# Kernel optimization log

Measured on AMD Instinct MI355X. Metric: run time of the kernel, lower is better.

## Reference

```python
import jax, jax.numpy as jnp
import numpy as np

VOCAB = 256; EMB = 384; D_MODEL = 512; D_INNER = 1024; D_STATE = 16
D_CONV = 4; DT_RANK = 32; NL = 8; B = 2; L = 2048

def silu(x):
    return x * jax.nn.sigmoid(x)

def layernorm(x, g, b):
    mu = x.mean(-1, keepdims=True)
    v = ((x - mu) ** 2).mean(-1, keepdims=True)
    return (x - mu) / jnp.sqrt(v + 1e-5) * g + b

def conv1d_same(x, w, b, pad):
    # x: (B, C, L), w: (O, I, K)
    out = jax.lax.conv_general_dilated(x, w, (1,), [(pad, pad)],
                                       dimension_numbers=('NCH', 'OIH', 'NCH'))
    return out + b[None, :, None]

def mamba_layer(x, in_w, cw, cb, xp_w, dt_w, dt_b, A_log, Dp, out_w):
    # x: (B, L, D_MODEL)
    xz = x @ in_w.T                      # (B, L, 2*D_INNER)
    xi, z = xz[..., :D_INNER], xz[..., D_INNER:]
    # causal depthwise conv over time
    xi_t = xi.transpose(0, 2, 1)         # (B, D_INNER, L)
    xc = jax.lax.conv_general_dilated(xi_t, cw[:, None, :], (1,), [(D_CONV - 1, 0)],
                                      dimension_numbers=('NCH', 'OIH', 'NCH'),
                                      feature_group_count=D_INNER)
    xc = silu(xc + cb[None, :, None]).transpose(0, 2, 1)   # (B, L, D_INNER)
    dbc = xc @ xp_w.T                    # (B, L, DT_RANK + 2*D_STATE)
    dt = jax.nn.softplus(dbc[..., :DT_RANK] @ dt_w.T + dt_b)   # (B, L, D_INNER)
    Bm = dbc[..., DT_RANK:DT_RANK + D_STATE]                    # (B, L, D_STATE)
    Cm = dbc[..., DT_RANK + D_STATE:]                           # (B, L, D_STATE)
    A = -jnp.exp(A_log)                                         # (D_INNER, D_STATE)
    dA = jnp.exp(dt[..., None] * A)                             # (B, L, D_INNER, D_STATE)
    dBx = (dt * xc)[..., None] * Bm[:, :, None, :]              # (B, L, D_INNER, D_STATE)

    def step(h, inp):
        a, bx, c = inp
        h = a * h + bx                                          # (B, D_INNER, D_STATE)
        return h, jnp.einsum('bds,bs->bd', h, c)

    h0 = jnp.zeros((x.shape[0], D_INNER, D_STATE), x.dtype)
    _, ys = jax.lax.scan(step, h0, (dA.transpose(1, 0, 2, 3),
                                    dBx.transpose(1, 0, 2, 3),
                                    Cm.transpose(1, 0, 2)))
    y = ys.transpose(1, 0, 2) + Dp * xc                         # (B, L, D_INNER)
    y = y * silu(z)
    return y @ out_w.T

def setup_inputs() -> dict:
    key = jax.random.key(0)
    ks = jax.random.split(key, 24)
    s = 0.02
    inp = {
        'tokens': jax.random.randint(ks[0], (B, L), 0, VOCAB),
        'emb': jax.random.normal(ks[1], (VOCAB, EMB)) * s,
        'conv1_w': jax.random.normal(ks[2], (512, EMB, 5)) * s,
        'conv1_b': jnp.zeros((512,)),
        'ln1_g': jnp.ones((512,)), 'ln1_b': jnp.zeros((512,)),
        'conv2_w': jax.random.normal(ks[3], (512, 512, 3)) * s,
        'conv2_b': jnp.zeros((512,)),
        'ln2_g': jnp.ones((512,)), 'ln2_b': jnp.zeros((512,)),
        'pos_emb': jax.random.normal(ks[4], (L, D_MODEL)) * s,
        'in_proj_w': jax.random.normal(ks[5], (NL, 2 * D_INNER, D_MODEL)) * s,
        'conv_w': jax.random.normal(ks[6], (NL, D_INNER, D_CONV)) * s,
        'conv_b': jnp.zeros((NL, D_INNER)),
        'x_proj_w': jax.random.normal(ks[7], (NL, DT_RANK + 2 * D_STATE, D_INNER)) * s,
        'dt_proj_w': jax.random.normal(ks[8], (NL, D_INNER, DT_RANK)) * s,
        'dt_proj_b': jnp.full((NL, D_INNER), -4.0),
        'A_log': jnp.log(jnp.tile(jnp.arange(1, D_STATE + 1, dtype=jnp.float32),
                                  (NL, D_INNER, 1))),
        'D': jnp.ones((NL, D_INNER)),
        'out_proj_w': jax.random.normal(ks[9], (NL, D_MODEL, D_INNER)) * s,
        'fc_w': jax.random.normal(ks[10], (VOCAB, D_MODEL)) * s,
        'fc_b': jnp.zeros((VOCAB,)),
    }
    return inp

def reference(tokens, emb, conv1_w, conv1_b, ln1_g, ln1_b, conv2_w, conv2_b,
              ln2_g, ln2_b, pos_emb, in_proj_w, conv_w, conv_b, x_proj_w,
              dt_proj_w, dt_proj_b, A_log, D, out_proj_w, fc_w, fc_b):
    x = emb[tokens]                                   # (B, L, EMB)
    # CNN frontend (GELU + channel LayerNorm, dropout=0 in eval)
    x = x.transpose(0, 2, 1)
    x = jax.nn.gelu(conv1d_same(x, conv1_w, conv1_b, 2), approximate=False)
    x = layernorm(x.transpose(0, 2, 1), ln1_g, ln1_b).transpose(0, 2, 1)
    x = jax.nn.gelu(conv1d_same(x, conv2_w, conv2_b, 1), approximate=False)
    x = layernorm(x.transpose(0, 2, 1), ln2_g, ln2_b)  # (B, L, 512)
    x = x + pos_emb[None, :x.shape[1]]
    for i in range(NL):
        x = mamba_layer(x, in_proj_w[i], conv_w[i], conv_b[i], x_proj_w[i],
                        dt_proj_w[i], dt_proj_b[i], A_log[i], D[i], out_proj_w[i])
    rep = x[:, -1, :]
    return rep @ fc_w.T + fc_b
```

## Files before the change

### kernel.cpp

```cpp
#include <hip/hip_runtime.h>
#include <hip/hip_bf16.h>
#include <math.h>

#define VOCABN 256
#define EMBN   384
#define DM     512
#define DI     1024
#define DSTATE 16
#define DCONVN 4
#define DTRANK 32
#define NLAYER 8
#define BBATCH 2
#define LSEQ   2048
#define MROWS  (BBATCH*LSEQ)
#define SCHUNK 64
#define NCHUNK (LSEQ/SCHUNK)

typedef short s8v  __attribute__((ext_vector_type(8)));
typedef float f32x4 __attribute__((ext_vector_type(4)));

__device__ __forceinline__ ushort f2bf(float f) {
    uint u = __float_as_uint(f);
    return (ushort)((u + 0x7fffu + ((u >> 16) & 1u)) >> 16);
}
__device__ __forceinline__ float bf2f(ushort h) {
    return __uint_as_float((uint)h << 16);
}
__device__ __forceinline__ uint packbf(float f) {
    ushort h = f2bf(f);
    ushort l = f2bf(f - bf2f(h));
    return ((uint)h << 16) | (uint)l;
}
__device__ __forceinline__ void unp4(uint4 p, ushort* hdst, ushort* ldst) {
    ushort4 h, l;
    h.x = (ushort)(p.x >> 16); l.x = (ushort)(p.x & 0xffffu);
    h.y = (ushort)(p.y >> 16); l.y = (ushort)(p.y & 0xffffu);
    h.z = (ushort)(p.z >> 16); l.z = (ushort)(p.z & 0xffffu);
    h.w = (ushort)(p.w >> 16); l.w = (ushort)(p.w & 0xffffu);
    *(ushort4*)hdst = h; *(ushort4*)ldst = l;
}

__global__ void pack3_kernel(const float* __restrict__ a, int na,
                             const float* __restrict__ b, int nb,
                             const float* __restrict__ c, int nc,
                             uint* __restrict__ pa, uint* __restrict__ pb, uint* __restrict__ pc) {
    int i = blockIdx.x * 256 + threadIdx.x;
    if (i < na) pa[i] = packbf(a[i]);
    else if (i < na + nb) pb[i - na] = packbf(b[i - na]);
    else if (i < na + nb + nc) pc[i - na - nb] = packbf(c[i - na - nb]);
}

template<int CI, int CK>
__global__ void pack_convw_kernel(const float* __restrict__ w, uint* __restrict__ pw) {
    int idx = blockIdx.x * 256 + threadIdx.x;
    if (idx >= 512 * CI * CK) return;
    int k  = idx % CK;
    int ci = (idx / CK) % CI;
    int co = idx / (CK * CI);
    pw[((size_t)(k * 512) + co) * CI + ci] = packbf(w[idx]);
}

__global__ void embed_kernel(const int* __restrict__ tok, const float* __restrict__ emb,
                             uint* __restrict__ px0) {
    int idx = blockIdx.x * 256 + threadIdx.x;
    int c = idx % EMBN;
    int t = idx / EMBN;
    px0[idx] = packbf(emb[tok[t] * EMBN + c]);
}

__device__ __forceinline__ float gelu_exact(float x) {
    return 0.5f * x * (1.f + erff(x * 0.70710678118654752f));
}

template<int CI, int CK, int PAD>
__global__ __launch_bounds__(256) void conv_mfma_kernel(
    const uint* __restrict__ PA, const uint* __restrict__ PW,
    const float* __restrict__ bias, float* __restrict__ out)
{
    constexpr int ROWS = 128 + CK - 1;
    const int t0  = blockIdx.x * 128;
    const int co0 = blockIdx.y * 32;
    const int tid = threadIdx.x;
    const int wid = tid >> 6, lane = tid & 63;
    const int rb = wid * 32;
    const int lr = lane & 15, lk = (lane >> 4) * 8;
    const int bstart = (t0 / LSEQ) * LSEQ;

    __shared__ alignas(16) ushort Ah[ROWS][40], Al[ROWS][40];
    __shared__ alignas(16) ushort Bh[CK][32][40], Bl[CK][32][40];

    f32x4 acc[2][2];
#pragma unroll
    for (int m = 0; m < 2; m++)
#pragma unroll
        for (int n = 0; n < 2; n++) acc[m][n] = (f32x4){0.f, 0.f, 0.f, 0.f};

    for (int ci0 = 0; ci0 < CI; ci0 += 32) {
        __syncthreads();
        for (int idx = tid; idx < ROWS * 8; idx += 256) {
            int r = idx >> 3, c4 = (idx & 7) * 4;
            int g = t0 - PAD + r;
            uint4 v = make_uint4(0u, 0u, 0u, 0u);
            if (g >= bstart && g < bstart + LSEQ)
                v = *(const uint4*)&PA[(size_t)g * CI + ci0 + c4];
            unp4(v, &Ah[r][c4], &Al[r][c4]);
        }
        for (int idx = tid; idx < CK * 32 * 8; idx += 256) {
            int k = idx >> 8;
            int r = (idx >> 3) & 31;
            int c4 = (idx & 7) * 4;
            uint4 v = *(const uint4*)&PW[((size_t)(k * 512) + co0 + r) * CI + ci0 + c4];
            unp4(v, &Bh[k][r][c4], &Bl[k][r][c4]);
        }
        __syncthreads();

#pragma unroll
        for (int k = 0; k < CK; k++) {
            s8v ah[2], al[2], bh[2], bl[2];
#pragma unroll
            for (int m = 0; m < 2; m++) {
                ah[m] = *(const s8v*)&Ah[rb + m * 16 + lr + k][lk];
                al[m] = *(const s8v*)&Al[rb + m * 16 + lr + k][lk];
            }
#pragma unroll
            for (int n = 0; n < 2; n++) {
                bh[n] = *(const s8v*)&Bh[k][n * 16 + lr][lk];
                bl[n] = *(const s8v*)&Bl[k][n * 16 + lr][lk];
            }
#pragma unroll
            for (int m = 0; m < 2; m++)
#pragma unroll
                for (int n = 0; n < 2; n++) {
                    acc[m][n] = __builtin_amdgcn_mfma_f32_16x16x32_bf16(ah[m], bh[n], acc[m][n], 0, 0, 0);
                    acc[m][n] = __builtin_amdgcn_mfma_f32_16x16x32_bf16(ah[m], bl[n], acc[m][n], 0, 0, 0);
                    acc[m][n] = __builtin_amdgcn_mfma_f32_16x16x32_bf16(al[m], bh[n], acc[m][n], 0, 0, 0);
                }
        }
    }

#pragma unroll
    for (int m = 0; m < 2; m++)
#pragma unroll
        for (int n = 0; n < 2; n++) {
            int gcol = co0 + n * 16 + lr;
            float bv = bias[gcol];
#pragma unroll
            for (int r = 0; r < 4; r++) {
                int grow = t0 + rb + m * 16 + (lane >> 4) * 4 + r;
                out[(size_t)grow * 512 + gcol] = gelu_exact(acc[m][n][r] + bv);
            }
        }
}

template<bool ADDPOS, bool PACK>
__global__ __launch_bounds__(256) void ln_kernel(
    const float* __restrict__ in, const float* __restrict__ g, const float* __restrict__ bb,
    const float* __restrict__ pos, float* __restrict__ out, uint* __restrict__ pout)
{
    int row  = blockIdx.x * 4 + (threadIdx.x >> 6);
    int lane = threadIdx.x & 63;
    const float* xr = in + (size_t)row * DM;
    float v[8];
    float s = 0.f;
#pragma unroll
    for (int i = 0; i < 8; i++) { v[i] = xr[lane + i * 64]; s += v[i]; }
#pragma unroll
    for (int o = 32; o >= 1; o >>= 1) s += __shfl_xor(s, o);
    float mu = s * (1.f / 512.f);
    float var = 0.f;
#pragma unroll
    for (int i = 0; i < 8; i++) { float d = v[i] - mu; var = fmaf(d, d, var); }
#pragma unroll
    for (int o = 32; o >= 1; o >>= 1) var += __shfl_xor(var, o);
    var *= (1.f / 512.f);
    float rstd = rsqrtf(var + 1e-5f);
    int t = row & (LSEQ - 1);
#pragma unroll
    for (int i = 0; i < 8; i++) {
        int c = lane + i * 64;
        float o = (v[i] - mu) * rstd * g[c] + bb[c];
        if (ADDPOS) o += pos[t * DM + c];
        if (PACK) pout[(size_t)row * DM + c] = packbf(o);
        else      out [(size_t)row * DM + c] = o;
    }
}

template<int EPI>
__global__ __launch_bounds__(256) void gemm_kernel(
    const float* __restrict__ A, int lda,
    const float* __restrict__ Wm,
    const float* __restrict__ bias,
    float* __restrict__ C, int N, int K)
{
    const int m0 = blockIdx.x * 64;
    const int n0 = blockIdx.y * 64;
    const int tid = threadIdx.x;
    const int tx = tid & 15, ty = tid >> 4;

    __shared__ float As[16][64];
    __shared__ float Ws[16][64];

    float acc[4][4];
#pragma unroll
    for (int i = 0; i < 4; i++)
#pragma unroll
        for (int j = 0; j < 4; j++) acc[i][j] = 0.f;

    const int am = tid >> 2;
    const int ak = (tid & 3) * 4;

    for (int k0 = 0; k0 < K; k0 += 16) {
        float4 av = *(const float4*)&A[(size_t)(m0 + am) * lda + k0 + ak];
        float4 wv = *(const float4*)&Wm[(size_t)(n0 + am) * K + k0 + ak];
        __syncthreads();
        As[ak + 0][am] = av.x; As[ak + 1][am] = av.y; As[ak + 2][am] = av.z; As[ak + 3][am] = av.w;
        Ws[ak + 0][am] = wv.x; Ws[ak + 1][am] = wv.y; Ws[ak + 2][am] = wv.z; Ws[ak + 3][am] = wv.w;
        __syncthreads();
#pragma unroll
        for (int kk = 0; kk < 16; kk++) {
            float4 a = *(const float4*)&As[kk][ty * 4];
            float4 w = *(const float4*)&Ws[kk][tx * 4];
            acc[0][0] = fmaf(a.x, w.x, acc[0][0]); acc[0][1] = fmaf(a.x, w.y, acc[0][1]);
            acc[0][2] = fmaf(a.x, w.z, acc[0][2]); acc[0][3] = fmaf(a.x, w.w, acc[0][3]);
            acc[1][0] = fmaf(a.y, w.x, acc[1][0]); acc[1][1] = fmaf(a.y, w.y, acc[1][1]);
            acc[1][2] = fmaf(a.y, w.z, acc[1][2]); acc[1][3] = fmaf(a.y, w.w, acc[1][3]);
            acc[2][0] = fmaf(a.z, w.x, acc[2][0]); acc[2][1] = fmaf(a.z, w.y, acc[2][1]);
            acc[2][2] = fmaf(a.z, w.z, acc[2][2]); acc[2][3] = fmaf(a.z, w.w, acc[2][3]);
            acc[3][0] = fmaf(a.w, w.x, acc[3][0]); acc[3][1] = fmaf(a.w, w.y, acc[3][1]);
            acc[3][2] = fmaf(a.w, w.z, acc[3][2]); acc[3][3] = fmaf(a.w, w.w, acc[3][3]);
        }
    }

#pragma unroll
    for (int i = 0; i < 4; i++) {
        float4 o;
        float r[4];
#pragma unroll
        for (int j = 0; j < 4; j++) {
            float v = acc[i][j];
            if (EPI == 1) {
                v += bias[n0 + tx * 4 + j];
                v = fmaxf(v, 0.f) + log1pf(expf(-fabsf(v)));
            }
            r[j] = v;
        }
        o.x = r[0]; o.y = r[1]; o.z = r[2]; o.w = r[3];
        *(float4*)&C[(size_t)(m0 + ty * 4 + i) * N + n0 + tx * 4] = o;
    }
}

template<int BN, int EPI>
__global__ __launch_bounds__(256) void gemm_mfma_p(
    const uint* __restrict__ PA, int lda,
    const uint* __restrict__ PW,
    float* __restrict__ C, uint* __restrict__ PC, int N, int K)
{
    constexpr int MR = (BN == 128) ? 4 : 2;
    constexpr int NR = 4;
    const int m0 = blockIdx.x * 128;
    const int n0 = blockIdx.y * BN;
    const int tid = threadIdx.x;
    const int wid = tid >> 6;
    const int lane = tid & 63;
    const int rb = (BN == 128) ? (wid >> 1) * 64 : wid * 32;
    const int cb = (BN == 128) ? (wid & 1) * 64 : 0;
    const int lr = lane & 15;
    const int lk = (lane >> 4) * 8;

    __shared__ alignas(16) ushort Ah[128][40], Al[128][40];
    __shared__ alignas(16) ushort Bh[BN][40],  Bl[BN][40];

    f32x4 acc[MR][NR];
#pragma unroll
    for (int m = 0; m < MR; m++)
#pragma unroll
        for (int n = 0; n < NR; n++) acc[m][n] = (f32x4){0.f, 0.f, 0.f, 0.f};

    const int srow = tid >> 3;
    const int scol = (tid & 7) * 4;

    for (int k0 = 0; k0 < K; k0 += 32) {
        uint4 av[4], wv[BN / 32];
#pragma unroll
        for (int i = 0; i < 4; i++)
            av[i] = *(const uint4*)&PA[(size_t)(m0 + srow + 32 * i) * lda + k0 + scol];
#pragma unroll
        for (int i = 0; i < BN / 32; i++)
            wv[i] = *(const uint4*)&PW[(size_t)(n0 + srow + 32 * i) * K + k0 + scol];

        __syncthreads();
#pragma unroll
        for (int i = 0; i < 4; i++)
            unp4(av[i], &Ah[srow + 32 * i][scol], &Al[srow + 32 * i][scol]);
#pragma unroll
        for (int i = 0; i < BN / 32; i++)
            unp4(wv[i], &Bh[srow + 32 * i][scol], &Bl[srow + 32 * i][scol]);
        __syncthreads();

        s8v ah[MR], al[MR], bh[NR], bl[NR];
#pragma unroll
        for (int m = 0; m < MR; m++) {
            ah[m] = *(const s8v*)&Ah[rb + m * 16 + lr][lk];
            al[m] = *(const s8v*)&Al[rb + m * 16 + lr][lk];
        }
#pragma unroll
        for (int n = 0; n < NR; n++) {
            bh[n] = *(const s8v*)&Bh[cb + n * 16 + lr][lk];
            bl[n] = *(const s8v*)&Bl[cb + n * 16 + lr][lk];
        }
#pragma unroll
        for (int m = 0; m < MR; m++)
#pragma unroll
            for (int n = 0; n < NR; n++) {
                acc[m][n] = __builtin_amdgcn_mfma_f32_16x16x32_bf16(ah[m], bh[n], acc[m][n], 0, 0, 0);
                acc[m][n] = __builtin_amdgcn_mfma_f32_16x16x32_bf16(ah[m], bl[n], acc[m][n], 0, 0, 0);
                acc[m][n] = __builtin_amdgcn_mfma_f32_16x16x32_bf16(al[m], bh[n], acc[m][n], 0, 0, 0);
            }
    }

#pragma unroll
    for (int m = 0; m < MR; m++)
#pragma unroll
        for (int n = 0; n < NR; n++) {
#pragma unroll
            for (int r = 0; r < 4; r++) {
                int grow = m0 + rb + m * 16 + (lane >> 4) * 4 + r;
                int gcol = n0 + cb + n * 16 + lr;
                float v = acc[m][n][r];
                C[(size_t)grow * N + gcol] = v;
                if (EPI == 2) PC[(size_t)grow * N + gcol] = packbf(v);
            }
        }
}

__global__ void dwconv_silu_kernel(const float* __restrict__ xz, const float* __restrict__ cw,
                                   const float* __restrict__ cb, float* __restrict__ xc,
                                   uint* __restrict__ pxc) {
    int idx = blockIdx.x * 256 + threadIdx.x;
    int d = idx & (DI - 1);
    int r = idx >> 10;
    int tl = r & (LSEQ - 1);
    float acc = cb[d];
#pragma unroll
    for (int k = 0; k < DCONVN; k++) {
        int ts = tl - 3 + k;
        if (ts >= 0) acc = fmaf(xz[(size_t)(r - 3 + k) * (2 * DI) + d], cw[d * DCONVN + k], acc);
    }
    float sig = 1.f / (1.f + expf(-acc));
    float v = acc * sig;
    xc[idx] = v;
    pxc[idx] = packbf(v);
}

__global__ __launch_bounds__(256) void scan_local_kernel(
    const float* __restrict__ dt, const float* __restrict__ xc,
    const float* __restrict__ dbc, const float* __restrict__ A_log,
    float* __restrict__ S, float* __restrict__ P)
{
    const int sg = threadIdx.x & 3;
    const int dl = threadIdx.x >> 2;
    const int dq = blockIdx.x & 15;
    const int c  = (blockIdx.x >> 4) & (NCHUNK - 1);
    const int b  = blockIdx.x >> 9;
    const int d  = dq * 64 + dl;

    float4 alog = *(const float4*)&A_log[d * DSTATE + sg * 4];
    float Av[4];
    Av[0] = -expf(alog.x) * 1.44269504f;
    Av[1] = -expf(alog.y) * 1.44269504f;
    Av[2] = -expf(alog.z) * 1.44269504f;
    Av[3] = -expf(alog.w) * 1.44269504f;

    float h[4] = {0.f, 0.f, 0.f, 0.f};
    float sumdt = 0.f;
    const int rowbase = b * LSEQ + c * SCHUNK;

#pragma unroll 4
    for (int t = 0; t < SCHUNK; t++) {
        int r = rowbase + t;
        float dtv = dt[(size_t)r * DI + d];
        float xcv = xc[(size_t)r * DI + d];
        float4 Bv = *(const float4*)&dbc[(size_t)r * 64 + DTRANK + sg * 4];
        float dx = dtv * xcv;
        h[0] = fmaf(exp2f(dtv * Av[0]), h[0], dx * Bv.x);
        h[1] = fmaf(exp2f(dtv * Av[1]), h[1], dx * Bv.y);
        h[2] = fmaf(exp2f(dtv * Av[2]), h[2], dx * Bv.z);
        h[3] = fmaf(exp2f(dtv * Av[3]), h[3], dx * Bv.w);
        sumdt += dtv;
    }
    size_t off = ((size_t)(b * NCHUNK + c) * DI + d) * DSTATE + sg * 4;
    *(float4*)&S[off] = make_float4(h[0], h[1], h[2], h[3]);
    *(float4*)&P[off] = make_float4(exp2f(Av[0] * sumdt), exp2f(Av[1] * sumdt),
                                    exp2f(Av[2] * sumdt), exp2f(Av[3] * sumdt));
}

__global__ __launch_bounds__(256) void scan_combine_kernel(
    const float* __restrict__ S, const float* __restrict__ P, float* __restrict__ H)
{
    int idx = blockIdx.x * 256 + threadIdx.x;
    int b = idx >> 14;
    int rem = idx & 16383;
    float h = 0.f;
#pragma unroll
    for (int c = 0; c < NCHUNK; c++) {
        size_t off = ((size_t)(b * NCHUNK + c) * DI) * DSTATE + rem;
        H[off] = h;
        h = fmaf(P[off], h, S[off]);
    }
}

__global__ __launch_bounds__(256) void scan_out_kernel(
    const float* __restrict__ dt, const float* __restrict__ xc,
    const float* __restrict__ dbc, const float* __restrict__ xz,
    const float* __restrict__ A_log, const float* __restrict__ Dp,
    const float* __restrict__ H, uint* __restrict__ py)
{
    const int sg = threadIdx.x & 3;
    const int dl = threadIdx.x >> 2;
    const int dq = blockIdx.x & 15;
    const int c  = (blockIdx.x >> 4) & (NCHUNK - 1);
    const int b  = blockIdx.x >> 9;
    const int d  = dq * 64 + dl;

    float4 alog = *(const float4*)&A_log[d * DSTATE + sg * 4];
    float Av[4];
    Av[0] = -expf(alog.x) * 1.44269504f;
    Av[1] = -expf(alog.y) * 1.44269504f;
    Av[2] = -expf(alog.z) * 1.44269504f;
    Av[3] = -expf(alog.w) * 1.44269504f;
    float Dval = Dp[d];

    float4 hv = *(const float4*)&H[((size_t)(b * NCHUNK + c) * DI + d) * DSTATE + sg * 4];
    float h[4] = {hv.x, hv.y, hv.z, hv.w};
    const int rowbase = b * LSEQ + c * SCHUNK;

#pragma unroll 2
    for (int t = 0; t < SCHUNK; t++) {
        int r = rowbase + t;
        float dtv = dt[(size_t)r * DI + d];
        float xcv = xc[(size_t)r * DI + d];
        float4 Bv = *(const float4*)&dbc[(size_t)r * 64 + DTRANK + sg * 4];
        float4 Cv = *(const float4*)&dbc[(size_t)r * 64 + DTRANK + DSTATE + sg * 4];
        float dx = dtv * xcv;
        h[0] = fmaf(exp2f(dtv * Av[0]), h[0], dx * Bv.x);
        h[1] = fmaf(exp2f(dtv * Av[1]), h[1], dx * Bv.y);
        h[2] = fmaf(exp2f(dtv * Av[2]), h[2], dx * Bv.z);
        h[3] = fmaf(exp2f(dtv * Av[3]), h[3], dx * Bv.w);
        float p = h[0] * Cv.x;
        p = fmaf(h[1], Cv.y, p);
        p = fmaf(h[2], Cv.z, p);
        p = fmaf(h[3], Cv.w, p);
        p += __shfl_xor(p, 1);
        p += __shfl_xor(p, 2);
        if (sg == 0) {
            float zv = xz[(size_t)r * (2 * DI) + DI + d];
            float zsig = 1.f / (1.f + exp2f(-zv * 1.44269504f));
            py[(size_t)r * DI + d] = packbf((p + Dval * xcv) * (zv * zsig));
        }
    }
}

__global__ void fc_kernel(const float* __restrict__ x, const float* __restrict__ fcw,
                          const float* __restrict__ fcb, float* __restrict__ out) {
    int b = blockIdx.x;
    int v = threadIdx.x;
    __shared__ float rep[DM];
    const float* xr = x + (size_t)(b * LSEQ + LSEQ - 1) * DM;
    for (int i = threadIdx.x; i < DM; i += 256) rep[i] = xr[i];
    __syncthreads();
    float acc = fcb[v];
    for (int k = 0; k < DM; k++) acc = fmaf(rep[k], fcw[v * DM + k], acc);
    out[b * VOCABN + v] = acc;
}

extern "C" void kernel_launch(void* const* d_in, const int* in_sizes, int n_in,
                              void* d_out, int out_size, void* d_ws, size_t ws_size,
                              hipStream_t stream) {
    const int*   tokens    = (const int*)  d_in[0];
    const float* emb       = (const float*)d_in[1];
    const float* conv1_w   = (const float*)d_in[2];
    const float* conv1_b   = (const float*)d_in[3];
    const float* ln1_g     = (const float*)d_in[4];
    const float* ln1_b     = (const float*)d_in[5];
    const float* conv2_w   = (const float*)d_in[6];
    const float* conv2_b   = (const float*)d_in[7];
    const float* ln2_g     = (const float*)d_in[8];
    const float* ln2_b     = (const float*)d_in[9];
    const float* pos_emb   = (const float*)d_in[10];
    const float* in_proj_w = (const float*)d_in[11];
    const float* conv_w    = (const float*)d_in[12];
    const float* conv_b    = (const float*)d_in[13];
    const float* x_proj_w  = (const float*)d_in[14];
    const float* dt_proj_w = (const float*)d_in[15];
    const float* dt_proj_b = (const float*)d_in[16];
    const float* A_log     = (const float*)d_in[17];
    const float* Dp_all    = (const float*)d_in[18];
    const float* out_proj_w= (const float*)d_in[19];
    const float* fc_w      = (const float*)d_in[20];
    const float* fc_b      = (const float*)d_in[21];

    float* ws = (float*)d_ws;
    float* X    = ws;
    float* T1   = X   + 2097152;
    float* XZ   = T1  + 2097152;
    float* XC   = XZ  + 8388608;
    float* DT   = XC  + 4194304;
    uint*  PY   = (uint*)(DT + 4194304);
    float* DBC  = (float*)PY + 4194304;
    uint*  PX   = (uint*)(DBC + 262144);
    uint*  PXC  = PX  + 2097152;
    uint*  PWIN = PXC + 4194304;
    uint*  PWOUT= PWIN + 1048576;
    uint*  PWX  = PWOUT + 524288;
    uint*  PX0  = (uint*)XZ;
    uint*  PWC1 = (uint*)XC;
    uint*  PWC2 = (uint*)XC + 983040;
    uint*  PB   = (uint*)DT;
    float* SCN_S = (float*)PXC;
    float* SCN_P = SCN_S + 1048576;
    float* SCN_H = SCN_P + 1048576;

    pack_convw_kernel<EMBN, 5><<<(512 * EMBN * 5 + 255) / 256, 256, 0, stream>>>(conv1_w, PWC1);
    pack_convw_kernel<DM,   3><<<(512 * DM   * 3 + 255) / 256, 256, 0, stream>>>(conv2_w, PWC2);
    embed_kernel<<<(MROWS * EMBN) / 256, 256, 0, stream>>>(tokens, emb, PX0);
    conv_mfma_kernel<EMBN, 5, 2><<<dim3(MROWS / 128, 16), 256, 0, stream>>>(PX0, PWC1, conv1_b, T1);
    ln_kernel<false, true><<<MROWS / 4, 256, 0, stream>>>(T1, ln1_g, ln1_b, nullptr, nullptr, PB);
    conv_mfma_kernel<DM, 3, 1><<<dim3(MROWS / 128, 16), 256, 0, stream>>>(PB, PWC2, conv2_b, T1);
    ln_kernel<true, true><<<MROWS / 4, 256, 0, stream>>>(T1, ln2_g, ln2_b, pos_emb, nullptr, PX);

    for (int l = 0; l < NLAYER; l++) {
        pack3_kernel<<<(2 * DI * DM + DM * DI + 64 * DI + 255) / 256, 256, 0, stream>>>(
            in_proj_w + (size_t)l * 2 * DI * DM, 2 * DI * DM,
            out_proj_w + (size_t)l * DM * DI, DM * DI,
            x_proj_w + (size_t)l * 64 * DI, 64 * DI,
            PWIN, PWOUT, PWX);
        gemm_mfma_p<128, 0><<<dim3(MROWS / 128, (2 * DI) / 128), 256, 0, stream>>>(
            PX, DM, PWIN, XZ, nullptr, 2 * DI, DM);
        dwconv_silu_kernel<<<(MROWS * DI) / 256, 256, 0, stream>>>(
            XZ, conv_w + (size_t)l * DI * DCONVN, conv_b + (size_t)l * DI, XC, PXC);
        gemm_mfma_p<64, 0><<<dim3(MROWS / 128, 1), 256, 0, stream>>>(
            PXC, DI, PWX, DBC, nullptr, 64, DI);
        gemm_kernel<1><<<dim3(MROWS / 64, DI / 64), 256, 0, stream>>>(
            DBC, 64, dt_proj_w + (size_t)l * DI * DTRANK, dt_proj_b + (size_t)l * DI, DT, DI, DTRANK);
        scan_local_kernel<<<16 * NCHUNK * BBATCH, 256, 0, stream>>>(
            DT, XC, DBC, A_log + (size_t)l * DI * DSTATE, SCN_S, SCN_P);
        scan_combine_kernel<<<(BBATCH * DI * DSTATE) / 256, 256, 0, stream>>>(
            SCN_S, SCN_P, SCN_H);
        scan_out_kernel<<<16 * NCHUNK * BBATCH, 256, 0, stream>>>(
            DT, XC, DBC, XZ, A_log + (size_t)l * DI * DSTATE, Dp_all + (size_t)l * DI,
            SCN_H, PY);
        gemm_mfma_p<64, 2><<<dim3(MROWS / 128, DM / 64), 256, 0, stream>>>(
            PY, DI, PWOUT, X, PX, DM, DI);
    }

    fc_kernel<<<BBATCH, 256, 0, stream>>>(X, fc_w, fc_b, (float*)d_out);
}
```

Measured before the change: 2.129 ms.

## Move dt projection to split-bf16 MFMA GEMM and stage scan inputs in LDS

Replaces the scalar fp32 dt_proj GEMM with the split-bf16 MFMA GEMM. Its weights are packed with the other layer weights, the x_proj output is packed as input, and bias plus softplus are fused in a new epilogue. The scan_local and scan_out kernels now preload each chunk's dt, xc and B/C rows into shared memory with vectorized loads instead of doing strided per-thread global reads each timestep. The risks are a K=32 GEMM that fits the MFMA K-loop tiling only loosely, and extra LDS use per block.

```diff
diff --git a/kernel.cpp b/kernel.cpp
--- a/kernel.cpp
+++ b/kernel.cpp
@@ -40,14 +40,17 @@
     *(ushort4*)hdst = h; *(ushort4*)ldst = l;
 }
 
-__global__ void pack3_kernel(const float* __restrict__ a, int na,
+__global__ void pack4_kernel(const float* __restrict__ a, int na,
                              const float* __restrict__ b, int nb,
                              const float* __restrict__ c, int nc,
-                             uint* __restrict__ pa, uint* __restrict__ pb, uint* __restrict__ pc) {
+                             const float* __restrict__ d, int nd,
+                             uint* __restrict__ pa, uint* __restrict__ pb,
+                             uint* __restrict__ pc, uint* __restrict__ pd) {
     int i = blockIdx.x * 256 + threadIdx.x;
     if (i < na) pa[i] = packbf(a[i]);
     else if (i < na + nb) pb[i - na] = packbf(b[i - na]);
     else if (i < na + nb + nc) pc[i - na - nb] = packbf(c[i - na - nb]);
+    else if (i < na + nb + nc + nd) pd[i - na - nb - nc] = packbf(d[i - na - nb - nc]);
 }
 
 template<int CI, int CK>
@@ -185,74 +188,11 @@
     }
 }
 
-template<int EPI>
-__global__ __launch_bounds__(256) void gemm_kernel(
-    const float* __restrict__ A, int lda,
-    const float* __restrict__ Wm,
-    const float* __restrict__ bias,
-    float* __restrict__ C, int N, int K)
-{
-    const int m0 = blockIdx.x * 64;
-    const int n0 = blockIdx.y * 64;
-    const int tid = threadIdx.x;
-    const int tx = tid & 15, ty = tid >> 4;
-
-    __shared__ float As[16][64];
-    __shared__ float Ws[16][64];
-
-    float acc[4][4];
-#pragma unroll
-    for (int i = 0; i < 4; i++)
-#pragma unroll
-        for (int j = 0; j < 4; j++) acc[i][j] = 0.f;
-
-    const int am = tid >> 2;
-    const int ak = (tid & 3) * 4;
-
-    for (int k0 = 0; k0 < K; k0 += 16) {
-        float4 av = *(const float4*)&A[(size_t)(m0 + am) * lda + k0 + ak];
-        float4 wv = *(const float4*)&Wm[(size_t)(n0 + am) * K + k0 + ak];
-        __syncthreads();
-        As[ak + 0][am] = av.x; As[ak + 1][am] = av.y; As[ak + 2][am] = av.z; As[ak + 3][am] = av.w;
-        Ws[ak + 0][am] = wv.x; Ws[ak + 1][am] = wv.y; Ws[ak + 2][am] = wv.z; Ws[ak + 3][am] = wv.w;
-        __syncthreads();
-#pragma unroll
-        for (int kk = 0; kk < 16; kk++) {
-            float4 a = *(const float4*)&As[kk][ty * 4];
-            float4 w = *(const float4*)&Ws[kk][tx * 4];
-            acc[0][0] = fmaf(a.x, w.x, acc[0][0]); acc[0][1] = fmaf(a.x, w.y, acc[0][1]);
-            acc[0][2] = fmaf(a.x, w.z, acc[0][2]); acc[0][3] = fmaf(a.x, w.w, acc[0][3]);
-            acc[1][0] = fmaf(a.y, w.x, acc[1][0]); acc[1][1] = fmaf(a.y, w.y, acc[1][1]);
-            acc[1][2] = fmaf(a.y, w.z, acc[1][2]); acc[1][3] = fmaf(a.y, w.w, acc[1][3]);
-            acc[2][0] = fmaf(a.z, w.x, acc[2][0]); acc[2][1] = fmaf(a.z, w.y, acc[2][1]);
-            acc[2][2] = fmaf(a.z, w.z, acc[2][2]); acc[2][3] = fmaf(a.z, w.w, acc[2][3]);
-            acc[3][0] = fmaf(a.w, w.x, acc[3][0]); acc[3][1] = fmaf(a.w, w.y, acc[3][1]);
-            acc[3][2] = fmaf(a.w, w.z, acc[3][2]); acc[3][3] = fmaf(a.w, w.w, acc[3][3]);
-        }
-    }
-
-#pragma unroll
-    for (int i = 0; i < 4; i++) {
-        float4 o;
-        float r[4];
-#pragma unroll
-        for (int j = 0; j < 4; j++) {
-            float v = acc[i][j];
-            if (EPI == 1) {
-                v += bias[n0 + tx * 4 + j];
-                v = fmaxf(v, 0.f) + log1pf(expf(-fabsf(v)));
-            }
-            r[j] = v;
-        }
-        o.x = r[0]; o.y = r[1]; o.z = r[2]; o.w = r[3];
-        *(float4*)&C[(size_t)(m0 + ty * 4 + i) * N + n0 + tx * 4] = o;
-    }
-}
-
 template<int BN, int EPI>
 __global__ __launch_bounds__(256) void gemm_mfma_p(
     const uint* __restrict__ PA, int lda,
     const uint* __restrict__ PW,
+    const float* __restrict__ bias,
     float* __restrict__ C, uint* __restrict__ PC, int N, int K)
 {
     constexpr int MR = (BN == 128) ? 4 : 2;
@@ -327,6 +267,10 @@
                 int grow = m0 + rb + m * 16 + (lane >> 4) * 4 + r;
                 int gcol = n0 + cb + n * 16 + lr;
                 float v = acc[m][n][r];
+                if (EPI == 3) {
+                    v += bias[gcol];
+                    v = fmaxf(v, 0.f) + log1pf(expf(-fabsf(v)));
+                }
                 C[(size_t)grow * N + gcol] = v;
                 if (EPI == 2) PC[(size_t)grow * N + gcol] = packbf(v);
             }
@@ -362,7 +306,23 @@
     const int dq = blockIdx.x & 15;
     const int c  = (blockIdx.x >> 4) & (NCHUNK - 1);
     const int b  = blockIdx.x >> 9;
-    const int d  = dq * 64 + dl;
+    const int d0 = dq * 64;
+    const int d  = d0 + dl;
+    const int rowbase = b * LSEQ + c * SCHUNK;
+
+    __shared__ float dtl[SCHUNK][68];
+    __shared__ float xcl[SCHUNK][68];
+    __shared__ float bl [SCHUNK][16];
+
+    for (int i = threadIdx.x; i < SCHUNK * 16; i += 256) {
+        int t = i >> 4, c4 = (i & 15) * 4;
+        *(float4*)&dtl[t][c4] = *(const float4*)&dt[(size_t)(rowbase + t) * DI + d0 + c4];
+        *(float4*)&xcl[t][c4] = *(const float4*)&xc[(size_t)(rowbase + t) * DI + d0 + c4];
+    }
+    for (int i = threadIdx.x; i < SCHUNK * 4; i += 256) {
+        int t = i >> 2, c4 = (i & 3) * 4;
+        *(float4*)&bl[t][c4] = *(const float4*)&dbc[(size_t)(rowbase + t) * 64 + DTRANK + c4];
+    }
 
     float4 alog = *(const float4*)&A_log[d * DSTATE + sg * 4];
     float Av[4];
@@ -373,14 +333,13 @@
 
     float h[4] = {0.f, 0.f, 0.f, 0.f};
     float sumdt = 0.f;
-    const int rowbase = b * LSEQ + c * SCHUNK;
+    __syncthreads();
 
 #pragma unroll 4
     for (int t = 0; t < SCHUNK; t++) {
-        int r = rowbase + t;
-        float dtv = dt[(size_t)r * DI + d];
-        float xcv = xc[(size_t)r * DI + d];
-        float4 Bv = *(const float4*)&dbc[(size_t)r * 64 + DTRANK + sg * 4];
+        float dtv = dtl[t][dl];
+        float xcv = xcl[t][dl];
+        float4 Bv = *(const float4*)&bl[t][sg * 4];
         float dx = dtv * xcv;
         h[0] = fmaf(exp2f(dtv * Av[0]), h[0], dx * Bv.x);
         h[1] = fmaf(exp2f(dtv * Av[1]), h[1], dx * Bv.y);
@@ -420,7 +379,23 @@
     const int dq = blockIdx.x & 15;
     const int c  = (blockIdx.x >> 4) & (NCHUNK - 1);
     const int b  = blockIdx.x >> 9;
-    const int d  = dq * 64 + dl;
+    const int d0 = dq * 64;
+    const int d  = d0 + dl;
+    const int rowbase = b * LSEQ + c * SCHUNK;
+
+    __shared__ float dtl[SCHUNK][68];
+    __shared__ float xcl[SCHUNK][68];
+    __shared__ float bcl[SCHUNK][32];
+
+    for (int i = threadIdx.x; i < SCHUNK * 16; i += 256) {
+        int t = i >> 4, c4 = (i & 15) * 4;
+        *(float4*)&dtl[t][c4] = *(const float4*)&dt[(size_t)(rowbase + t) * DI + d0 + c4];
+        *(float4*)&xcl[t][c4] = *(const float4*)&xc[(size_t)(rowbase + t) * DI + d0 + c4];
+    }
+    for (int i = threadIdx.x; i < SCHUNK * 8; i += 256) {
+        int t = i >> 3, c4 = (i & 7) * 4;
+        *(float4*)&bcl[t][c4] = *(const float4*)&dbc[(size_t)(rowbase + t) * 64 + DTRANK + c4];
+    }
 
     float4 alog = *(const float4*)&A_log[d * DSTATE + sg * 4];
     float Av[4];
@@ -432,15 +407,14 @@
 
     float4 hv = *(const float4*)&H[((size_t)(b * NCHUNK + c) * DI + d) * DSTATE + sg * 4];
     float h[4] = {hv.x, hv.y, hv.z, hv.w};
-    const int rowbase = b * LSEQ + c * SCHUNK;
-
-#pragma unroll 2
+    __syncthreads();
+
+#pragma unroll 4
     for (int t = 0; t < SCHUNK; t++) {
-        int r = rowbase + t;
-        float dtv = dt[(size_t)r * DI + d];
-        float xcv = xc[(size_t)r * DI + d];
-        float4 Bv = *(const float4*)&dbc[(size_t)r * 64 + DTRANK + sg * 4];
-        float4 Cv = *(const float4*)&dbc[(size_t)r * 64 + DTRANK + DSTATE + sg * 4];
+        float dtv = dtl[t][dl];
+        float xcv = xcl[t][dl];
+        float4 Bv = *(const float4*)&bcl[t][sg * 4];
+        float4 Cv = *(const float4*)&bcl[t][16 + sg * 4];
         float dx = dtv * xcv;
         h[0] = fmaf(exp2f(dtv * Av[0]), h[0], dx * Bv.x);
         h[1] = fmaf(exp2f(dtv * Av[1]), h[1], dx * Bv.y);
@@ -453,9 +427,9 @@
         p += __shfl_xor(p, 1);
         p += __shfl_xor(p, 2);
         if (sg == 0) {
-            float zv = xz[(size_t)r * (2 * DI) + DI + d];
+            float zv = xz[(size_t)(rowbase + t) * (2 * DI) + DI + d];
             float zsig = 1.f / (1.f + exp2f(-zv * 1.44269504f));
-            py[(size_t)r * DI + d] = packbf((p + Dval * xcv) * (zv * zsig));
+            py[(size_t)(rowbase + t) * DI + d] = packbf((p + Dval * xcv) * (zv * zsig));
         }
     }
 }
@@ -512,6 +486,8 @@
     uint*  PWIN = PXC + 4194304;
     uint*  PWOUT= PWIN + 1048576;
     uint*  PWX  = PWOUT + 524288;
+    uint*  PWDT = PWX + 65536;
+    uint*  PDBC = PWDT + 32768;
     uint*  PX0  = (uint*)XZ;
     uint*  PWC1 = (uint*)XC;
     uint*  PWC2 = (uint*)XC + 983040;
@@ -528,20 +504,22 @@
     conv_mfma_kernel<DM, 3, 1><<<dim3(MROWS / 128, 16), 256, 0, stream>>>(PB, PWC2, conv2_b, T1);
     ln_kernel<true, true><<<MROWS / 4, 256, 0, stream>>>(T1, ln2_g, ln2_b, pos_emb, nullptr, PX);
 
+    const int NPACK = 2 * DI * DM + DM * DI + 64 * DI + DI * DTRANK;
     for (int l = 0; l < NLAYER; l++) {
-        pack3_kernel<<<(2 * DI * DM + DM * DI + 64 * DI + 255) / 256, 256, 0, stream>>>(
+        pack4_kernel<<<(NPACK + 255) / 256, 256, 0, stream>>>(
             in_proj_w + (size_t)l * 2 * DI * DM, 2 * DI * DM,
             out_proj_w + (size_t)l * DM * DI, DM * DI,
             x_proj_w + (size_t)l * 64 * DI, 64 * DI,
-            PWIN, PWOUT, PWX);
+            dt_proj_w + (size_t)l * DI * DTRANK, DI * DTRANK,
+            PWIN, PWOUT, PWX, PWDT);
         gemm_mfma_p<128, 0><<<dim3(MROWS / 128, (2 * DI) / 128), 256, 0, stream>>>(
-            PX, DM, PWIN, XZ, nullptr, 2 * DI, DM);
+            PX, DM, PWIN, nullptr, XZ, nullptr, 2 * DI, DM);
         dwconv_silu_kernel<<<(MROWS * DI) / 256, 256, 0, stream>>>(
             XZ, conv_w + (size_t)l * DI * DCONVN, conv_b + (size_t)l * DI, XC, PXC);
-        gemm_mfma_p<64, 0><<<dim3(MROWS / 128, 1), 256, 0, stream>>>(
-            PXC, DI, PWX, DBC, nullptr, 64, DI);
-        gemm_kernel<1><<<dim3(MROWS / 64, DI / 64), 256, 0, stream>>>(
-            DBC, 64, dt_proj_w + (size_t)l * DI * DTRANK, dt_proj_b + (size_t)l * DI, DT, DI, DTRANK);
+        gemm_mfma_p<64, 2><<<dim3(MROWS / 128, 1), 256, 0, stream>>>(
+            PXC, DI, PWX, nullptr, DBC, PDBC, 64, DI);
+        gemm_mfma_p<128, 3><<<dim3(MROWS / 128, DI / 128), 256, 0, stream>>>(
+            PDBC, 64, PWDT, dt_proj_b + (size_t)l * DI, DT, nullptr, DI, DTRANK);
         scan_local_kernel<<<16 * NCHUNK * BBATCH, 256, 0, stream>>>(
             DT, XC, DBC, A_log + (size_t)l * DI * DSTATE, SCN_S, SCN_P);
         scan_combine_kernel<<<(BBATCH * DI * DSTATE) / 256, 256, 0, stream>>>(
@@ -550,7 +528,7 @@
             DT, XC, DBC, XZ, A_log + (size_t)l * DI * DSTATE, Dp_all + (size_t)l * DI,
             SCN_H, PY);
         gemm_mfma_p<64, 2><<<dim3(MROWS / 128, DM / 64), 256, 0, stream>>>(
-            PY, DI, PWOUT, X, PX, DM, DI);
+            PY, DI, PWOUT, nullptr, X, PX, DM, DI);
     }
 
     fc_kernel<<<BBATCH, 256, 0, stream>>>(X, fc_w, fc_b, (float*)d_out);
```

Measured after the change: 2.300 ms. 8.1% more time.
